# Kernel optimization log

Measured on AMD Instinct MI355X. Metric: run time of the kernel, lower is better.

Reference implementation:

```python
import jax, jax.numpy as jnp
import numpy as np

B, S, D, H = 2, 2048, 1024, 16
DEPTH = D // H


def setup_inputs() -> dict:
    key = jax.random.key(0)
    ks = jax.random.split(key, 9)
    sc = 1.0 / np.sqrt(D)
    return {
        "x": jax.random.normal(ks[0], (B, S, D), dtype=jnp.float32),
        "wq": jax.random.normal(ks[1], (D, D), dtype=jnp.float32) * sc,
        "bq": jnp.zeros((D,), dtype=jnp.float32),
        "wk": jax.random.normal(ks[2], (D, D), dtype=jnp.float32) * sc,
        "bk": jnp.zeros((D,), dtype=jnp.float32),
        "wv": jax.random.normal(ks[3], (D, D), dtype=jnp.float32) * sc,
        "bv": jnp.zeros((D,), dtype=jnp.float32),
        "wo": jax.random.normal(ks[4], (D, D), dtype=jnp.float32) * sc,
        "bo": jnp.zeros((D,), dtype=jnp.float32),
    }


def _split_heads(t):
    # [B,S,D] -> [B,H,S,depth]
    return t.reshape(B, S, H, DEPTH).transpose(0, 2, 1, 3)


def reference(x, wq, bq, wk, bk, wv, bv, wo, bo):
    q = _split_heads(x @ wq + bq)
    k = _split_heads(x @ wk + bk)
    v = _split_heads(x @ wv + bv)
    scale = 1.0 / jnp.sqrt(jnp.asarray(DEPTH, dtype=x.dtype))
    logits = jnp.einsum("bhqd,bhkd->bhqk", q, k) * scale
    attn = jax.nn.relu(logits)  # ReLU replaces softmax
    ctx = jnp.einsum("bhqk,bhkd->bhqd", attn, v)
    concat = ctx.transpose(0, 2, 1, 3).reshape(B, S, D)
    out = concat @ wo + bo
    return out, attn
```

## Files before the change

kernel.cpp:

```cpp
#include <hip/hip_runtime.h>
#include <hip/hip_bf16.h>

constexpr int Bn = 2, Sn = 2048, Dn = 1024, Hn = 16, DEP = 64;
constexpr int NTOKn = Bn * Sn;

typedef __bf16 bf16x8 __attribute__((ext_vector_type(8)));
typedef float f32x4 __attribute__((ext_vector_type(4)));

__device__ __forceinline__ unsigned short f2bf(float f) {
    union { __hip_bfloat16 h; unsigned short u; } cv;
    cv.h = __float2bfloat16(f);
    return cv.u;
}

__device__ __forceinline__ void gll16(const void* g, void* l) {
    __builtin_amdgcn_global_load_lds(
        (const __attribute__((address_space(1))) unsigned int*)g,
        (__attribute__((address_space(3))) unsigned int*)l, 16, 0, 0);
}

__global__ __launch_bounds__(256) void k_prep(const float* __restrict__ x,
                                              const float* __restrict__ w0,
                                              const float* __restrict__ w1,
                                              const float* __restrict__ w2,
                                              const float* __restrict__ w3,
                                              unsigned short* __restrict__ xb,
                                              unsigned short* __restrict__ t0,
                                              unsigned short* __restrict__ t1,
                                              unsigned short* __restrict__ t2,
                                              unsigned short* __restrict__ t3) {
    const int bid = blockIdx.x;
    const int t = threadIdx.x;
    if (bid < 4096) {
        const int idx = (bid * 256 + t) * 4;
        float4 v = *reinterpret_cast<const float4*>(x + idx);
        ushort4 o;
        o.x = f2bf(v.x); o.y = f2bf(v.y); o.z = f2bf(v.z); o.w = f2bf(v.w);
        *reinterpret_cast<ushort4*>(xb + idx) = o;
        return;
    }
    const int b2 = bid - 4096;
    const float* w; unsigned short* tp;
    switch (b2 >> 8) {
        case 0: w = w0; tp = t0; break;
        case 1: w = w1; tp = t1; break;
        case 2: w = w2; tp = t2; break;
        default: w = w3; tp = t3; break;
    }
    __shared__ unsigned short tile[64][65];
    const int k0 = ((b2 & 255) >> 4) * 64, n0 = (b2 & 15) * 64;
    const int c = t & 63, rb = t >> 6;
#pragma unroll
    for (int i = 0; i < 16; ++i) {
        int r = rb + i * 4;
        tile[r][c] = f2bf(w[(size_t)(k0 + r) * Dn + n0 + c]);
    }
    __syncthreads();
#pragma unroll
    for (int i = 0; i < 16; ++i) {
        int n = rb + i * 4;
        tp[(size_t)(n0 + n) * Dn + k0 + c] = tile[c][n];
    }
}

__global__ __launch_bounds__(256) void k_tr_v(const unsigned short* __restrict__ V,
                                              unsigned short* __restrict__ VT) {
    __shared__ unsigned short tile[64][65];
    const int s0 = blockIdx.x * 64;
    const int bh = blockIdx.y;
    const int b = bh >> 4, h = bh & 15;
    const int t = threadIdx.x;
    const int c = t & 63, rb = t >> 6;
#pragma unroll
    for (int i = 0; i < 16; ++i) {
        int r = rb + i * 4;
        tile[r][c] = V[(size_t)(b * Sn + s0 + r) * Dn + h * DEP + c];
    }
    __syncthreads();
#pragma unroll
    for (int i = 0; i < 16; ++i) {
        int d = rb + i * 4;
        VT[(size_t)(bh * DEP + d) * Sn + s0 + c] = tile[c][d];
    }
}

__global__ __launch_bounds__(512, 2) void k_qkv8(const unsigned short* __restrict__ A,
                                                 const unsigned short* __restrict__ Bt,
                                                 const float* __restrict__ bq,
                                                 const float* __restrict__ bk,
                                                 const float* __restrict__ bv,
                                                 unsigned short* __restrict__ qkv) {
    extern __shared__ char smem[];
    constexpr int K = 1024, NT = K / 64;

    const int t = threadIdx.x;
    const int w = t >> 6, l = t & 63;
    const int wm = w >> 2, wn = w & 3;
    const int m0 = blockIdx.x * 256;
    const int n0 = blockIdx.y * 256;
    const int z = n0 >> 10;

    const float* bias = (z == 0) ? bq : (z == 1 ? bk : bv);
    float biasv[4];
#pragma unroll
    for (int nf = 0; nf < 4; ++nf)
        biasv[nf] = bias[(n0 + wn * 64 + nf * 16 + (l & 15)) & 1023];

    int aoff[2], boff[2], ldsoff[2];
#pragma unroll
    for (int i = 0; i < 2; ++i) {
        const int idx = i * 512 + t;
        const int row = idx >> 2;
        const int s = ((idx & 3) - row - (row >> 2)) & 3;
        aoff[i] = (m0 + row) * K + s * 8;
        boff[i] = (n0 + row) * K + s * 8;
        ldsoff[i] = idx * 16;
    }

    f32x4 acc[8][4] = {};

#pragma unroll
    for (int kh = 0; kh < 2; ++kh) {
        if (kh == 0) {
#pragma unroll
            for (int i = 0; i < 2; ++i) gll16(A + aoff[i], smem + ldsoff[i]);
#pragma unroll
            for (int i = 0; i < 2; ++i) gll16(Bt + boff[i], smem + 65536 + ldsoff[i]);
        } else {
#pragma unroll
            for (int i = 0; i < 2; ++i) gll16(A + aoff[i] + 32, smem + 16384 + ldsoff[i]);
#pragma unroll
            for (int i = 0; i < 2; ++i) gll16(Bt + boff[i] + 32, smem + 65536 + 16384 + ldsoff[i]);
        }
    }

    for (int kb = 0; kb < NT; ++kb) {
        const int c = kb & 1;
        const int kn = (kb + 1 < NT) ? kb + 1 : NT - 1;
        const int cn = c ^ 1;
        const int Abase = c * 32768;
        const int Bbase = 65536 + c * 32768;
        const int AbaseN = cn * 32768;
        const int BbaseN = 65536 + cn * 32768;

        bf16x8 bf[4], af[4];

#pragma unroll
        for (int ph = 0; ph < 4; ++ph) {
            const int kk = ph >> 1;
            const int mb = (ph & 1) * 4;

            if ((ph & 1) == 0) {
                asm volatile("s_waitcnt vmcnt(4)" ::: "memory");
            }
            __builtin_amdgcn_s_barrier();
            __builtin_amdgcn_sched_barrier(0);

            if ((ph & 1) == 0) {
#pragma unroll
                for (int nf = 0; nf < 4; ++nf) {
                    const int row = wn * 64 + nf * 16 + (l & 15);
                    const int byte = Bbase + kk * 16384 + row * 64 +
                                     ((((l >> 4) + row + (row >> 2)) & 3) * 16);
                    bf[nf] = *reinterpret_cast<const bf16x8*>(smem + byte);
                }
            }
#pragma unroll
            for (int mfl = 0; mfl < 4; ++mfl) {
                const int row = wm * 128 + (mb + mfl) * 16 + (l & 15);
                const int byte = Abase + kk * 16384 + row * 64 +
                                 ((((l >> 4) + row + (row >> 2)) & 3) * 16);
                af[mfl] = *reinterpret_cast<const bf16x8*>(smem + byte);
            }

            {
                const int khs = ph >> 1;
                if ((ph & 1) == 0) {
#pragma unroll
                    for (int i = 0; i < 2; ++i)
                        gll16(A + aoff[i] + kn * 64 + khs * 32,
                              smem + AbaseN + khs * 16384 + ldsoff[i]);
                } else {
#pragma unroll
                    for (int i = 0; i < 2; ++i)
                        gll16(Bt + boff[i] + kn * 64 + khs * 32,
                              smem + BbaseN + khs * 16384 + ldsoff[i]);
                }
            }

            asm volatile("s_waitcnt lgkmcnt(0)" ::: "memory");
            __builtin_amdgcn_sched_barrier(0);
            __builtin_amdgcn_s_setprio(1);
#pragma unroll
            for (int mfl = 0; mfl < 4; ++mfl)
#pragma unroll
                for (int nf = 0; nf < 4; ++nf)
                    acc[mb + mfl][nf] = __builtin_amdgcn_mfma_f32_16x16x32_bf16(
                        af[mfl], bf[nf], acc[mb + mfl][nf], 0, 0, 0);
            __builtin_amdgcn_s_setprio(0);
        }
    }

    asm volatile("s_waitcnt vmcnt(0)" ::: "memory");

    unsigned short* outz = qkv + (size_t)z * NTOKn * Dn;
#pragma unroll
    for (int mf = 0; mf < 8; ++mf) {
        const int row = m0 + wm * 128 + mf * 16 + (l >> 4) * 4;
#pragma unroll
        for (int nf = 0; nf < 4; ++nf) {
            const int col = (n0 + wn * 64 + nf * 16 + (l & 15)) & 1023;
#pragma unroll
            for (int i = 0; i < 4; ++i)
                outz[(size_t)(row + i) * Dn + col] = f2bf(acc[mf][nf][i] + biasv[nf]);
        }
    }
}

__global__ __launch_bounds__(256) void k_gemm_op(const unsigned short* __restrict__ A,
                                                 const unsigned short* __restrict__ Bt,
                                                 const float* __restrict__ bias,
                                                 float* __restrict__ C,
                                                 int M, int N, int K) {
    __shared__ unsigned short As[128][32];
    __shared__ unsigned short Bs[128][32];
    const int t = threadIdx.x;
    const int w = t >> 6, l = t & 63;
    const int m0 = blockIdx.x * 128, n0 = blockIdx.y * 128;
    const int wr = (w >> 1) * 64, wc = (w & 1) * 64;

    const int lrow = t >> 2;
    const int lcol = (t & 3) * 8;
    const unsigned short* gA = A + (size_t)(m0 + lrow) * K + lcol;
    const unsigned short* gB = Bt + (size_t)(n0 + lrow) * K + lcol;
    unsigned short* lA = &As[0][0] + t * 8;
    unsigned short* lB = &Bs[0][0] + t * 8;

    f32x4 acc[4][4] = {};

    for (int k0 = 0; k0 < K; k0 += 32) {
        __syncthreads();
        gll16(gA + k0, lA);
        gll16(gA + (size_t)64 * K + k0, lA + 2048);
        gll16(gB + k0, lB);
        gll16(gB + (size_t)64 * K + k0, lB + 2048);
        __syncthreads();

        bf16x8 af[4], bfv[4];
#pragma unroll
        for (int i = 0; i < 4; ++i)
            af[i] = *reinterpret_cast<const bf16x8*>(&As[wr + i * 16 + (l & 15)][(l >> 4) * 8]);
#pragma unroll
        for (int i = 0; i < 4; ++i)
            bfv[i] = *reinterpret_cast<const bf16x8*>(&Bs[wc + i * 16 + (l & 15)][(l >> 4) * 8]);
#pragma unroll
        for (int mi = 0; mi < 4; ++mi)
#pragma unroll
            for (int ni = 0; ni < 4; ++ni)
                acc[mi][ni] =
                    __builtin_amdgcn_mfma_f32_16x16x32_bf16(af[mi], bfv[ni], acc[mi][ni], 0, 0, 0);
    }

#pragma unroll
    for (int mi = 0; mi < 4; ++mi) {
        const int row = m0 + wr + mi * 16 + (l >> 4) * 4;
#pragma unroll
        for (int ni = 0; ni < 4; ++ni) {
            const int col = n0 + wc + ni * 16 + (l & 15);
            const float bv = bias[col];
#pragma unroll
            for (int i = 0; i < 4; ++i)
                C[(size_t)(row + i) * N + col] = acc[mi][ni][i] + bv;
        }
    }
}

__global__ __launch_bounds__(256, 2) void k_attn(const unsigned short* __restrict__ Qb,
                                                 const unsigned short* __restrict__ Kb,
                                                 const unsigned short* __restrict__ VTb,
                                                 float* __restrict__ attn,
                                                 unsigned short* __restrict__ ctx) {
    __shared__ unsigned short Ks[128 * 64];
    __shared__ unsigned short Vs[64 * 128];
    __shared__ unsigned short Ps[4][32][136];

    const int t = threadIdx.x;
    const int w = t >> 6, l = t & 63;

    const int lin = blockIdx.x + 16 * blockIdx.y;
    const int xcd = lin & 7, idx = lin >> 3;
    const int bh = xcd * 4 + (idx >> 4);
    const int q0 = (idx & 15) * 128;
    const int b = bh >> 4, h = bh & 15;
    const float scale = 0.125f;

    bf16x8 qf[2][2];
#pragma unroll
    for (int mi = 0; mi < 2; ++mi)
#pragma unroll
        for (int kk = 0; kk < 2; ++kk)
            qf[mi][kk] = *reinterpret_cast<const bf16x8*>(
                Qb + (size_t)(b * Sn + q0 + w * 32 + mi * 16 + (l & 15)) * Dn + h * DEP +
                kk * 32 + (l >> 4) * 8);

    const int krow = t >> 3;
    const int kcolswz = ((t & 7) * 8) ^ ((krow & 7) << 3);
    const int vrow = t >> 4;
    const int vcolswz = ((t & 15) * 8) ^ ((vrow & 7) << 3);
    unsigned short* lK = Ks + t * 8;
    unsigned short* lV = Vs + t * 8;

    f32x4 ctxa[2][4] = {};
    f32x4 sa[2][8];

    float* const abase = attn + (size_t)bh * Sn * Sn + (size_t)(q0 + w * 32) * Sn;

    auto STAGE = [&](int kb) {
#pragma unroll
        for (int is = 0; is < 4; ++is) {
            gll16(Kb + (size_t)(b * Sn + kb * 128 + is * 32 + krow) * Dn + h * DEP + kcolswz,
                  lK + is * 2048);
            gll16(VTb + (size_t)(bh * DEP + is * 16 + vrow) * Sn + kb * 128 + vcolswz,
                  lV + is * 2048);
        }
    };

    auto QKT = [&]() {
#pragma unroll
        for (int mi = 0; mi < 2; ++mi)
#pragma unroll
            for (int nj = 0; nj < 8; ++nj)
                sa[mi][nj] = (f32x4){0.f, 0.f, 0.f, 0.f};
#pragma unroll
        for (int nj = 0; nj < 8; ++nj) {
            const int kr = nj * 16 + (l & 15);
#pragma unroll
            for (int kk = 0; kk < 2; ++kk) {
                const int kidx = (kr * 64 + kk * 32 + (l >> 4) * 8) ^ ((kr & 7) << 3);
                const bf16x8 bfr = *reinterpret_cast<const bf16x8*>(Ks + kidx);
                sa[0][nj] = __builtin_amdgcn_mfma_f32_16x16x32_bf16(qf[0][kk], bfr, sa[0][nj], 0, 0, 0);
                sa[1][nj] = __builtin_amdgcn_mfma_f32_16x16x32_bf16(qf[1][kk], bfr, sa[1][nj], 0, 0, 0);
            }
        }
#pragma unroll
        for (int mi = 0; mi < 2; ++mi) {
#pragma unroll
            for (int nj = 0; nj < 8; ++nj) {
                f32x4 v = sa[mi][nj];
#pragma unroll
                for (int i = 0; i < 4; ++i) {
                    float p = v[i] * scale;
                    v[i] = p > 0.f ? p : 0.f;
                }
                sa[mi][nj] = v;
                const int kc = nj * 16 + (l & 15);
#pragma unroll
                for (int i = 0; i < 4; ++i)
                    Ps[w][mi * 16 + (l >> 4) * 4 + i][kc] = f2bf(v[i]);
            }
        }
    };

    auto PV = [&]() {
        bf16x8 pf[2][4];
#pragma unroll
        for (int mi = 0; mi < 2; ++mi)
#pragma unroll
            for (int kk = 0; kk < 4; ++kk)
                pf[mi][kk] = *reinterpret_cast<const bf16x8*>(
                    &Ps[w][mi * 16 + (l & 15)][kk * 32 + (l >> 4) * 8]);
#pragma unroll
        for (int nd = 0; nd < 4; ++nd) {
            const int vr = nd * 16 + (l & 15);
#pragma unroll
            for (int kk = 0; kk < 4; ++kk) {
                const int vidx = (vr * 128 + kk * 32 + (l >> 4) * 8) ^ ((vr & 7) << 3);
                const bf16x8 vfr = *reinterpret_cast<const bf16x8*>(Vs + vidx);
                ctxa[0][nd] = __builtin_amdgcn_mfma_f32_16x16x32_bf16(pf[0][kk], vfr, ctxa[0][nd], 0, 0, 0);
                ctxa[1][nd] = __builtin_amdgcn_mfma_f32_16x16x32_bf16(pf[1][kk], vfr, ctxa[1][nd], 0, 0, 0);
            }
        }
    };

    auto STORE_SA = [&](int kb) {
        float* arow = abase + kb * 128;
#pragma unroll
        for (int mi = 0; mi < 2; ++mi)
#pragma unroll
            for (int nj = 0; nj < 8; ++nj) {
                const int kc = nj * 16 + (l & 15);
#pragma unroll
                for (int i = 0; i < 4; ++i)
                    arow[(size_t)(mi * 16 + (l >> 4) * 4 + i) * Sn + kc] = sa[mi][nj][i];
            }
    };

    STAGE(0);
    asm volatile("s_waitcnt vmcnt(0)" ::: "memory");
    __builtin_amdgcn_s_barrier();
    __builtin_amdgcn_sched_barrier(0);
    QKT();
    PV();

    for (int kb = 1; kb < Sn / 128; ++kb) {
        asm volatile("s_waitcnt lgkmcnt(0)" ::: "memory");
        __builtin_amdgcn_s_barrier();
        __builtin_amdgcn_sched_barrier(0);
        STAGE(kb);
        asm volatile("" ::: "memory");
        STORE_SA(kb - 1);
        asm volatile("s_waitcnt vmcnt(63)" ::: "memory");
        __builtin_amdgcn_s_barrier();
        __builtin_amdgcn_sched_barrier(0);
        QKT();
        PV();
    }
    STORE_SA(Sn / 128 - 1);

#pragma unroll
    for (int mi = 0; mi < 2; ++mi) {
#pragma unroll
        for (int nd = 0; nd < 4; ++nd) {
            const int dc = nd * 16 + (l & 15);
#pragma unroll
            for (int i = 0; i < 4; ++i) {
                const int qr = q0 + w * 32 + mi * 16 + (l >> 4) * 4 + i;
                ctx[(size_t)(b * Sn + qr) * Dn + h * DEP + dc] = f2bf(ctxa[mi][nd][i]);
            }
        }
    }
}

extern "C" void kernel_launch(void* const* d_in, const int* in_sizes, int n_in,
                              void* d_out, int out_size, void* d_ws, size_t ws_size,
                              hipStream_t stream) {
    (void)in_sizes; (void)n_in; (void)out_size; (void)ws_size;
    const float* x  = (const float*)d_in[0];
    const float* wq = (const float*)d_in[1];
    const float* bq = (const float*)d_in[2];
    const float* wk = (const float*)d_in[3];
    const float* bk = (const float*)d_in[4];
    const float* wv = (const float*)d_in[5];
    const float* bv = (const float*)d_in[6];
    const float* wo = (const float*)d_in[7];
    const float* bo = (const float*)d_in[8];

    float* out  = (float*)d_out;
    float* attn = out + (size_t)Bn * Sn * Dn;

    char* ws = (char*)d_ws;
    unsigned short* xb = (unsigned short*)ws;  ws += (size_t)NTOKn * Dn * 2;
    unsigned short* wT = (unsigned short*)ws;  ws += (size_t)4 * Dn * Dn * 2;
    unsigned short* qkv = (unsigned short*)ws; ws += (size_t)3 * NTOKn * Dn * 2;
    unsigned short* vT = (unsigned short*)ws;  ws += (size_t)NTOKn * Dn * 2;
    unsigned short* ctx = (unsigned short*)ws;

    const size_t DD = (size_t)Dn * Dn;

    static bool attr_set = false;
    if (!attr_set) {
        hipFuncSetAttribute(reinterpret_cast<const void*>(k_qkv8),
                            hipFuncAttributeMaxDynamicSharedMemorySize, 131072);
        attr_set = true;
    }

    k_prep<<<dim3(5120), 256, 0, stream>>>(x, wq, wk, wv, wo, xb,
                                           wT, wT + DD, wT + 2 * DD, wT + 3 * DD);
    k_qkv8<<<dim3(16, 12), 512, 131072, stream>>>(xb, wT, bq, bk, bv, qkv);
    k_tr_v<<<dim3(32, 32), 256, 0, stream>>>(qkv + (size_t)2 * NTOKn * Dn, vT);
    k_attn<<<dim3(16, 32), 256, 0, stream>>>(qkv, qkv + (size_t)NTOKn * Dn, vT, attn, ctx);
    k_gemm_op<<<dim3(32, 8), 256, 0, stream>>>(ctx, wT + 3 * DD, bo, out, NTOKn, Dn, Dn);
}
```

Baseline: 216.1 us.

## Fuse V transpose into QKV epilogue and use pipelined 256x256 output GEMM

The QKV GEMM epilogue now writes the V third directly in transposed [B,H,depth,S] layout with 4-element vector stores, which removes the separate transpose kernel and its extra round trip through memory. The simple 128x128 output-projection GEMM is replaced by a copy of the double-buffered, swizzled 256x256 pipelined kernel. The large tiles launch only 64 blocks for the output GEMM, which may leave many compute units idle. The transposed V stores are strided across rows of length S.

```diff
diff --git a/kernel.cpp b/kernel.cpp
--- a/kernel.cpp
+++ b/kernel.cpp
@@ -63,33 +63,13 @@
     }
 }
 
-__global__ __launch_bounds__(256) void k_tr_v(const unsigned short* __restrict__ V,
-                                              unsigned short* __restrict__ VT) {
-    __shared__ unsigned short tile[64][65];
-    const int s0 = blockIdx.x * 64;
-    const int bh = blockIdx.y;
-    const int b = bh >> 4, h = bh & 15;
-    const int t = threadIdx.x;
-    const int c = t & 63, rb = t >> 6;
-#pragma unroll
-    for (int i = 0; i < 16; ++i) {
-        int r = rb + i * 4;
-        tile[r][c] = V[(size_t)(b * Sn + s0 + r) * Dn + h * DEP + c];
-    }
-    __syncthreads();
-#pragma unroll
-    for (int i = 0; i < 16; ++i) {
-        int d = rb + i * 4;
-        VT[(size_t)(bh * DEP + d) * Sn + s0 + c] = tile[c][d];
-    }
-}
-
 __global__ __launch_bounds__(512, 2) void k_qkv8(const unsigned short* __restrict__ A,
                                                  const unsigned short* __restrict__ Bt,
                                                  const float* __restrict__ bq,
                                                  const float* __restrict__ bk,
                                                  const float* __restrict__ bv,
-                                                 unsigned short* __restrict__ qkv) {
+                                                 unsigned short* __restrict__ qkv,
+                                                 unsigned short* __restrict__ vT) {
     extern __shared__ char smem[];
     constexpr int K = 1024, NT = K / 64;
 
@@ -203,74 +183,162 @@
 
     asm volatile("s_waitcnt vmcnt(0)" ::: "memory");
 
-    unsigned short* outz = qkv + (size_t)z * NTOKn * Dn;
+    if (z < 2) {
+        unsigned short* outz = qkv + (size_t)z * NTOKn * Dn;
+#pragma unroll
+        for (int mf = 0; mf < 8; ++mf) {
+            const int row = m0 + wm * 128 + mf * 16 + (l >> 4) * 4;
+#pragma unroll
+            for (int nf = 0; nf < 4; ++nf) {
+                const int col = (n0 + wn * 64 + nf * 16 + (l & 15)) & 1023;
+#pragma unroll
+                for (int i = 0; i < 4; ++i)
+                    outz[(size_t)(row + i) * Dn + col] = f2bf(acc[mf][nf][i] + biasv[nf]);
+            }
+        }
+    } else {
+#pragma unroll
+        for (int mf = 0; mf < 8; ++mf) {
+            const int row = m0 + wm * 128 + mf * 16 + (l >> 4) * 4;
+            const int b = row >> 11, s = row & 2047;
+#pragma unroll
+            for (int nf = 0; nf < 4; ++nf) {
+                const int col = (n0 + wn * 64 + nf * 16 + (l & 15)) & 1023;
+                ushort4 o;
+                o.x = f2bf(acc[mf][nf][0] + biasv[nf]);
+                o.y = f2bf(acc[mf][nf][1] + biasv[nf]);
+                o.z = f2bf(acc[mf][nf][2] + biasv[nf]);
+                o.w = f2bf(acc[mf][nf][3] + biasv[nf]);
+                *reinterpret_cast<ushort4*>(vT + ((size_t)(b * 1024 + col)) * Sn + s) = o;
+            }
+        }
+    }
+}
+
+__global__ __launch_bounds__(512, 2) void k_op8(const unsigned short* __restrict__ A,
+                                                const unsigned short* __restrict__ Bt,
+                                                const float* __restrict__ bias,
+                                                float* __restrict__ C) {
+    extern __shared__ char smem[];
+    constexpr int K = 1024, NT = K / 64, N = 1024;
+
+    const int t = threadIdx.x;
+    const int w = t >> 6, l = t & 63;
+    const int wm = w >> 2, wn = w & 3;
+    const int m0 = blockIdx.x * 256;
+    const int n0 = blockIdx.y * 256;
+
+    float biasv[4];
+#pragma unroll
+    for (int nf = 0; nf < 4; ++nf)
+        biasv[nf] = bias[n0 + wn * 64 + nf * 16 + (l & 15)];
+
+    int aoff[2], boff[2], ldsoff[2];
+#pragma unroll
+    for (int i = 0; i < 2; ++i) {
+        const int idx = i * 512 + t;
+        const int row = idx >> 2;
+        const int s = ((idx & 3) - row - (row >> 2)) & 3;
+        aoff[i] = (m0 + row) * K + s * 8;
+        boff[i] = (n0 + row) * K + s * 8;
+        ldsoff[i] = idx * 16;
+    }
+
+    f32x4 acc[8][4] = {};
+
+#pragma unroll
+    for (int kh = 0; kh < 2; ++kh) {
+        if (kh == 0) {
+#pragma unroll
+            for (int i = 0; i < 2; ++i) gll16(A + aoff[i], smem + ldsoff[i]);
+#pragma unroll
+            for (int i = 0; i < 2; ++i) gll16(Bt + boff[i], smem + 65536 + ldsoff[i]);
+        } else {
+#pragma unroll
+            for (int i = 0; i < 2; ++i) gll16(A + aoff[i] + 32, smem + 16384 + ldsoff[i]);
+#pragma unroll
+            for (int i = 0; i < 2; ++i) gll16(Bt + boff[i] + 32, smem + 65536 + 16384 + ldsoff[i]);
+        }
+    }
+
+    for (int kb = 0; kb < NT; ++kb) {
+        const int c = kb & 1;
+        const int kn = (kb + 1 < NT) ? kb + 1 : NT - 1;
+        const int cn = c ^ 1;
+        const int Abase = c * 32768;
+        const int Bbase = 65536 + c * 32768;
+        const int AbaseN = cn * 32768;
+        const int BbaseN = 65536 + cn * 32768;
+
+        bf16x8 bf[4], af[4];
+
+#pragma unroll
+        for (int ph = 0; ph < 4; ++ph) {
+            const int kk = ph >> 1;
+            const int mb = (ph & 1) * 4;
+
+            if ((ph & 1) == 0) {
+                asm volatile("s_waitcnt vmcnt(4)" ::: "memory");
+            }
+            __builtin_amdgcn_s_barrier();
+            __builtin_amdgcn_sched_barrier(0);
+
+            if ((ph & 1) == 0) {
+#pragma unroll
+                for (int nf = 0; nf < 4; ++nf) {
+                    const int row = wn * 64 + nf * 16 + (l & 15);
+                    const int byte = Bbase + kk * 16384 + row * 64 +
+                                     ((((l >> 4) + row + (row >> 2)) & 3) * 16);
+                    bf[nf] = *reinterpret_cast<const bf16x8*>(smem + byte);
+                }
+            }
+#pragma unroll
+            for (int mfl = 0; mfl < 4; ++mfl) {
+                const int row = wm * 128 + (mb + mfl) * 16 + (l & 15);
+                const int byte = Abase + kk * 16384 + row * 64 +
+                                 ((((l >> 4) + row + (row >> 2)) & 3) * 16);
+                af[mfl] = *reinterpret_cast<const bf16x8*>(smem + byte);
+            }
+
+            {
+                const int khs = ph >> 1;
+                if ((ph & 1) == 0) {
+#pragma unroll
+                    for (int i = 0; i < 2; ++i)
+                        gll16(A + aoff[i] + kn * 64 + khs * 32,
+                              smem + AbaseN + khs * 16384 + ldsoff[i]);
+                } else {
+#pragma unroll
+                    for (int i = 0; i < 2; ++i)
+                        gll16(Bt + boff[i] + kn * 64 + khs * 32,
+                              smem + BbaseN + khs * 16384 + ldsoff[i]);
+                }
+            }
+
+            asm volatile("s_waitcnt lgkmcnt(0)" ::: "memory");
+            __builtin_amdgcn_sched_barrier(0);
+            __builtin_amdgcn_s_setprio(1);
+#pragma unroll
+            for (int mfl = 0; mfl < 4; ++mfl)
+#pragma unroll
+                for (int nf = 0; nf < 4; ++nf)
+                    acc[mb + mfl][nf] = __builtin_amdgcn_mfma_f32_16x16x32_bf16(
+                        af[mfl], bf[nf], acc[mb + mfl][nf], 0, 0, 0);
+            __builtin_amdgcn_s_setprio(0);
+        }
+    }
+
+    asm volatile("s_waitcnt vmcnt(0)" ::: "memory");
+
 #pragma unroll
     for (int mf = 0; mf < 8; ++mf) {
         const int row = m0 + wm * 128 + mf * 16 + (l >> 4) * 4;
 #pragma unroll
         for (int nf = 0; nf < 4; ++nf) {
-            const int col = (n0 + wn * 64 + nf * 16 + (l & 15)) & 1023;
+            const int col = n0 + wn * 64 + nf * 16 + (l & 15);
 #pragma unroll
             for (int i = 0; i < 4; ++i)
-                outz[(size_t)(row + i) * Dn + col] = f2bf(acc[mf][nf][i] + biasv[nf]);
-        }
-    }
-}
-
-__global__ __launch_bounds__(256) void k_gemm_op(const unsigned short* __restrict__ A,
-                                                 const unsigned short* __restrict__ Bt,
-                                                 const float* __restrict__ bias,
-                                                 float* __restrict__ C,
-                                                 int M, int N, int K) {
-    __shared__ unsigned short As[128][32];
-    __shared__ unsigned short Bs[128][32];
-    const int t = threadIdx.x;
-    const int w = t >> 6, l = t & 63;
-    const int m0 = blockIdx.x * 128, n0 = blockIdx.y * 128;
-    const int wr = (w >> 1) * 64, wc = (w & 1) * 64;
-
-    const int lrow = t >> 2;
-    const int lcol = (t & 3) * 8;
-    const unsigned short* gA = A + (size_t)(m0 + lrow) * K + lcol;
-    const unsigned short* gB = Bt + (size_t)(n0 + lrow) * K + lcol;
-    unsigned short* lA = &As[0][0] + t * 8;
-    unsigned short* lB = &Bs[0][0] + t * 8;
-
-    f32x4 acc[4][4] = {};
-
-    for (int k0 = 0; k0 < K; k0 += 32) {
-        __syncthreads();
-        gll16(gA + k0, lA);
-        gll16(gA + (size_t)64 * K + k0, lA + 2048);
-        gll16(gB + k0, lB);
-        gll16(gB + (size_t)64 * K + k0, lB + 2048);
-        __syncthreads();
-
-        bf16x8 af[4], bfv[4];
-#pragma unroll
-        for (int i = 0; i < 4; ++i)
-            af[i] = *reinterpret_cast<const bf16x8*>(&As[wr + i * 16 + (l & 15)][(l >> 4) * 8]);
-#pragma unroll
-        for (int i = 0; i < 4; ++i)
-            bfv[i] = *reinterpret_cast<const bf16x8*>(&Bs[wc + i * 16 + (l & 15)][(l >> 4) * 8]);
-#pragma unroll
-        for (int mi = 0; mi < 4; ++mi)
-#pragma unroll
-            for (int ni = 0; ni < 4; ++ni)
-                acc[mi][ni] =
-                    __builtin_amdgcn_mfma_f32_16x16x32_bf16(af[mi], bfv[ni], acc[mi][ni], 0, 0, 0);
-    }
-
-#pragma unroll
-    for (int mi = 0; mi < 4; ++mi) {
-        const int row = m0 + wr + mi * 16 + (l >> 4) * 4;
-#pragma unroll
-        for (int ni = 0; ni < 4; ++ni) {
-            const int col = n0 + wc + ni * 16 + (l & 15);
-            const float bv = bias[col];
-#pragma unroll
-            for (int i = 0; i < 4; ++i)
-                C[(size_t)(row + i) * N + col] = acc[mi][ni][i] + bv;
+                C[(size_t)(row + i) * N + col] = acc[mf][nf][i] + biasv[nf];
         }
     }
 }
@@ -461,13 +529,14 @@
     if (!attr_set) {
         hipFuncSetAttribute(reinterpret_cast<const void*>(k_qkv8),
                             hipFuncAttributeMaxDynamicSharedMemorySize, 131072);
+        hipFuncSetAttribute(reinterpret_cast<const void*>(k_op8),
+                            hipFuncAttributeMaxDynamicSharedMemorySize, 131072);
         attr_set = true;
     }
 
     k_prep<<<dim3(5120), 256, 0, stream>>>(x, wq, wk, wv, wo, xb,
                                            wT, wT + DD, wT + 2 * DD, wT + 3 * DD);
-    k_qkv8<<<dim3(16, 12), 512, 131072, stream>>>(xb, wT, bq, bk, bv, qkv);
-    k_tr_v<<<dim3(32, 32), 256, 0, stream>>>(qkv + (size_t)2 * NTOKn * Dn, vT);
+    k_qkv8<<<dim3(16, 12), 512, 131072, stream>>>(xb, wT, bq, bk, bv, qkv, vT);
     k_attn<<<dim3(16, 32), 256, 0, stream>>>(qkv, qkv + (size_t)NTOKn * Dn, vT, attn, ctx);
-    k_gemm_op<<<dim3(32, 8), 256, 0, stream>>>(ctx, wT + 3 * DD, bo, out, NTOKn, Dn, Dn);
-}
+    k_op8<<<dim3(16, 4), 512, 131072, stream>>>(ctx, wT + 3 * DD, bo, out);
+}
```

Result: no change. 215.4 us (-0.3%).
